# Performance work log

Measured on AMD Instinct MI355X. Metric: run time of the kernel, lower is better.

Reference implementation:

```python
import jax, jax.numpy as jnp
import numpy as np

B, N, N_IN, N_HID, EIN = 8, 256, 64, 128, 16


def setup_inputs() -> dict:
    key = jax.random.key(0)
    ks = jax.random.split(key, 12)
    s_in = 1.0 / np.sqrt(N_IN)
    s_e = 1.0 / np.sqrt(EIN)
    s_h = 1.0 / np.sqrt(N_HID)
    return {
        "x": jax.random.normal(ks[0], (B, N, N_IN), jnp.float32),
        "e": jax.random.normal(ks[1], (B, N, N, EIN), jnp.float32),
        "Wf": jax.random.uniform(ks[2], (N_IN, N_HID), jnp.float32, -s_in, s_in),
        "bf": jax.random.uniform(ks[3], (N_HID,), jnp.float32, -s_in, s_in),
        "Wt": jax.random.uniform(ks[4], (N_IN, N_HID), jnp.float32, -s_in, s_in),
        "bt": jax.random.uniform(ks[5], (N_HID,), jnp.float32, -s_in, s_in),
        "We": jax.random.uniform(ks[6], (EIN, N_HID), jnp.float32, -s_e, s_e),
        "be": jax.random.uniform(ks[7], (N_HID,), jnp.float32, -s_e, s_e),
        "W1": jax.random.uniform(ks[8], (N_HID, N_HID), jnp.float32, -s_h, s_h),
        "b1": jax.random.uniform(ks[9], (N_HID,), jnp.float32, -s_h, s_h),
        "W2": jax.random.uniform(ks[10], (N_HID, N_IN), jnp.float32, -s_h, s_h),
        "b2": jax.random.uniform(ks[11], (N_IN,), jnp.float32, -s_h, s_h),
    }


def reference(x, e, Wf, bf, Wt, bt, We, be, W1, b1, W2, b2):
    # x: [B,N,F], e: [B,N,N,E]
    n = x.shape[1]
    ne_f = x @ Wf + bf                      # [B,N,H] (node_emb_1)
    ne_t = x @ Wt + bt                      # [B,N,H] (node_emb_2)
    ee = e @ We + be                        # [B,N,N,H]
    # pair[b,i,j] = node_emb_1[b,j] + node_emb_2[b,i] + edge_emb[b,i,j]
    pair = ne_f[:, None, :, :] + ne_t[:, :, None, :] + ee
    # zero the diagonal (both node_emb and edge_emb diagonals were zeroed)
    mask = (1.0 - jnp.eye(n, dtype=x.dtype))[None, :, :, None]
    node_emb = jax.nn.relu(pair * mask).mean(axis=2)  # [B,N,H]
    h = jax.nn.relu(node_emb @ W1 + b1)
    return h @ W2 + b2 + x
```

## Files before the change

### kernel.cpp

```cpp
#include <hip/hip_runtime.h>
#include <hip/hip_bf16.h>


#define BB 8
#define NN 256
#define FF 64
#define HH 128
#define EE 16
#define NCH 5

typedef __attribute__((ext_vector_type(8))) short bf16x8;
typedef __attribute__((ext_vector_type(16))) float f32x16;

__device__ __forceinline__ short f2bf(float f) {
    union { float f; unsigned u; } v; v.f = f;
    unsigned r = v.u + 0x7FFFu + ((v.u >> 16) & 1u);
    return (short)(r >> 16);
}
__device__ __forceinline__ float bf2f(short s) {
    union { unsigned u; float f; } v; v.u = ((unsigned)(unsigned short)s) << 16;
    return v.f;
}
__device__ __forceinline__ unsigned pkbf(float lo, float hi) {
    unsigned r;
    asm("v_cvt_pk_bf16_f32 %0, %1, %2" : "=v"(r) : "v"(lo), "v"(hi));
    return r;
}
union bfu { bf16x8 v; unsigned u[4]; };

__global__ __launch_bounds__(128) void k_prep(
    const float* __restrict__ x, const float* __restrict__ Wt,
    const float* __restrict__ bf, const float* __restrict__ bt, const float* __restrict__ be,
    const float* __restrict__ We, const float* __restrict__ Wf,
    const float* __restrict__ W1, const float* __restrict__ W2,
    float* __restrict__ net, short* __restrict__ xbf,
    short* __restrict__ Bpack, short* __restrict__ W1p, short* __restrict__ W2p)
{
    __shared__ float smx[4 * FF];
    const int tid = threadIdx.x;
    const int row0 = blockIdx.x * 4;

    smx[tid]       = x[(size_t)row0 * FF + tid];
    smx[tid + 128] = x[(size_t)row0 * FF + tid + 128];
    __syncthreads();

    const int h = tid;
    const float bsum = bf[h] + bt[h] + be[h];
    float a0 = bsum, a1 = bsum, a2 = bsum, a3 = bsum;

    #pragma unroll 8
    for (int k = 0; k < FF; ++k) {
        const float wt = Wt[k * HH + h];
        a0 = fmaf(smx[k], wt, a0);
        a1 = fmaf(smx[FF + k], wt, a1);
        a2 = fmaf(smx[2 * FF + k], wt, a2);
        a3 = fmaf(smx[3 * FF + k], wt, a3);
    }
    net[(size_t)(row0 + 0) * HH + h] = a0;
    net[(size_t)(row0 + 1) * HH + h] = a1;
    net[(size_t)(row0 + 2) * HH + h] = a2;
    net[(size_t)(row0 + 3) * HH + h] = a3;

    const int r = tid >> 6, f = tid & 63;
    xbf[(size_t)(row0 + r) * FF + f]     = f2bf(smx[r * FF + f]);
    xbf[(size_t)(row0 + r + 2) * FF + f] = f2bf(smx[(r + 2) * FF + f]);

    if (blockIdx.x < 32) {
        for (int t = blockIdx.x * 128 + tid; t < 34816; t += 32 * 128) {
            if (t < 10240) {
                const int el = t & 7, lane = (t >> 3) & 63, ht = (t >> 9) & 3, ch = t >> 11;
                const int kl = 8 * (lane >> 5) + el;
                const int hh = ht * 32 + (lane & 31);
                Bpack[t] = f2bf(ch == 0 ? We[kl * HH + hh] : Wf[(16 * (ch - 1) + kl) * HH + hh]);
            } else if (t < 26624) {
                const int t2 = t - 10240;
                const int el = t2 & 7, lane = (t2 >> 3) & 63, ht = (t2 >> 9) & 3, ch = (t2 >> 11) & 7;
                const int k = 16 * ch + 8 * (lane >> 5) + el;
                const int hh = ht * 32 + (lane & 31);
                W1p[t2] = f2bf(W1[k * HH + hh]);
            } else {
                const int t3 = t - 26624;
                const int el = t3 & 7, lane = (t3 >> 3) & 63, ht = (t3 >> 9) & 1, ch = t3 >> 10;
                const int k = 16 * ch + 8 * (lane >> 5) + el;
                const int hh = ht * 32 + (lane & 31);
                W2p[t3] = f2bf(W2[k * FF + hh]);
            }
        }
    }
}

__global__ __launch_bounds__(256) void k_pair(
    const float* __restrict__ e, const float* __restrict__ net,
    const short* __restrict__ xbf, const short* __restrict__ Bpack,
    float* __restrict__ S)
{
    const int row  = blockIdx.x;
    const int b    = row >> 8;
    const int tid  = threadIdx.x;
    const int wave = tid >> 6;
    const int lane = tid & 63;
    const int c    = lane & 31;
    const int half = lane >> 5;

    const bf16x8* __restrict__ bp = (const bf16x8*)Bpack;
    bf16x8 bfrag[NCH];
    #pragma unroll
    for (int ch = 0; ch < NCH; ++ch)
        bfrag[ch] = bp[(ch * 4 + wave) * 64 + lane];

    const float netv = net[(size_t)row * HH + wave * 32 + c];

    const float* __restrict__ eRow = e + (size_t)row * (NN * EE);
    const short* __restrict__ xb   = xbf + (size_t)b * (NN * FF);

    float acc = 0.f;

    #pragma unroll 2
    for (int jt = 0; jt < 8; ++jt) {
        const int j = jt * 32 + c;

        const float4* ap = (const float4*)(eRow + (size_t)j * EE + 8 * half);
        const float4 p0 = ap[0];
        const float4 p1 = ap[1];
        bfu ae;
        ae.u[0] = pkbf(p0.x, p0.y);
        ae.u[1] = pkbf(p0.z, p0.w);
        ae.u[2] = pkbf(p1.x, p1.y);
        ae.u[3] = pkbf(p1.z, p1.w);

        const bf16x8* xp = (const bf16x8*)(xb + (size_t)j * FF + 8 * half);
        const bf16x8 ax0 = xp[0];
        const bf16x8 ax1 = xp[2];
        const bf16x8 ax2 = xp[4];
        const bf16x8 ax3 = xp[6];

        f32x16 d = {netv,netv,netv,netv, netv,netv,netv,netv,
                    netv,netv,netv,netv, netv,netv,netv,netv};
        d = __builtin_amdgcn_mfma_f32_32x32x16_bf16(ae.v, bfrag[0], d, 0, 0, 0);
        d = __builtin_amdgcn_mfma_f32_32x32x16_bf16(ax0,  bfrag[1], d, 0, 0, 0);
        d = __builtin_amdgcn_mfma_f32_32x32x16_bf16(ax1,  bfrag[2], d, 0, 0, 0);
        d = __builtin_amdgcn_mfma_f32_32x32x16_bf16(ax2,  bfrag[3], d, 0, 0, 0);
        d = __builtin_amdgcn_mfma_f32_32x32x16_bf16(ax3,  bfrag[4], d, 0, 0, 0);
        #pragma unroll
        for (int r = 0; r < 16; ++r) acc += fmaxf(d[r], 0.f);
    }

    acc += __shfl_xor(acc, 32);
    if (lane < 32) S[(size_t)row * HH + wave * 32 + c] = acc;
}

__global__ __launch_bounds__(256) void k_mlp(
    const float* __restrict__ x, const float* __restrict__ e,
    const float* __restrict__ S, const float* __restrict__ net,
    const short* __restrict__ xbf, const short* __restrict__ Bpack,
    const short* __restrict__ W1p, const short* __restrict__ W2p,
    const float* __restrict__ b1, const float* __restrict__ b2,
    float* __restrict__ out)
{
    const int row0 = blockIdx.x * 32;
    const int tid  = threadIdx.x;
    const int wave = tid >> 6;
    const int lane = tid & 63;
    const int c    = lane & 31;
    const int half = lane >> 5;

    __shared__ float Dt[32][132];
    __shared__ short neL[32][136];
    __shared__ short h1L[32][136];

    {
        const int gr = row0 + c;
        const int bb = gr >> 8, ii = gr & (NN - 1);
        const float* ed = e + ((size_t)(bb * NN + ii) * NN + ii) * EE + 8 * half;
        const float4 p0 = ((const float4*)ed)[0];
        const float4 p1 = ((const float4*)ed)[1];
        bfu ae;
        ae.u[0] = pkbf(p0.x, p0.y);
        ae.u[1] = pkbf(p0.z, p0.w);
        ae.u[2] = pkbf(p1.x, p1.y);
        ae.u[3] = pkbf(p1.z, p1.w);

        const bf16x8* xp = (const bf16x8*)(xbf + (size_t)gr * FF + 8 * half);
        const bf16x8 ax0 = xp[0];
        const bf16x8 ax1 = xp[2];
        const bf16x8 ax2 = xp[4];
        const bf16x8 ax3 = xp[6];

        const bf16x8* bp = (const bf16x8*)Bpack;
        f32x16 d = {0.f,0.f,0.f,0.f, 0.f,0.f,0.f,0.f, 0.f,0.f,0.f,0.f, 0.f,0.f,0.f,0.f};
        d = __builtin_amdgcn_mfma_f32_32x32x16_bf16(ae.v, bp[(0*4+wave)*64+lane], d, 0, 0, 0);
        d = __builtin_amdgcn_mfma_f32_32x32x16_bf16(ax0,  bp[(1*4+wave)*64+lane], d, 0, 0, 0);
        d = __builtin_amdgcn_mfma_f32_32x32x16_bf16(ax1,  bp[(2*4+wave)*64+lane], d, 0, 0, 0);
        d = __builtin_amdgcn_mfma_f32_32x32x16_bf16(ax2,  bp[(3*4+wave)*64+lane], d, 0, 0, 0);
        d = __builtin_amdgcn_mfma_f32_32x32x16_bf16(ax3,  bp[(4*4+wave)*64+lane], d, 0, 0, 0);
        #pragma unroll
        for (int r = 0; r < 16; ++r) {
            const int rowj = (r & 3) + 8 * (r >> 2) + 4 * half;
            Dt[rowj][wave * 32 + c] = d[r];
        }
    }
    __syncthreads();

    {
        const int r  = tid >> 3;
        const int h0 = (tid & 7) * 16;
        const size_t base = (size_t)(row0 + r) * HH + h0;
        unsigned uo[8];
        #pragma unroll
        for (int q = 0; q < 4; ++q) {
            const float4 sv = *(const float4*)&S[base + 4 * q];
            const float4 nv = *(const float4*)&net[base + 4 * q];
            const float4 dv = *(const float4*)&Dt[r][h0 + 4 * q];
            const float n0 = (sv.x - fmaxf(dv.x + nv.x, 0.f)) * (1.0f / NN);
            const float n1 = (sv.y - fmaxf(dv.y + nv.y, 0.f)) * (1.0f / NN);
            const float n2 = (sv.z - fmaxf(dv.z + nv.z, 0.f)) * (1.0f / NN);
            const float n3 = (sv.w - fmaxf(dv.w + nv.w, 0.f)) * (1.0f / NN);
            uo[2 * q]     = pkbf(n0, n1);
            uo[2 * q + 1] = pkbf(n2, n3);
        }
        uint4* dst = (uint4*)&neL[r][h0];
        dst[0] = make_uint4(uo[0], uo[1], uo[2], uo[3]);
        dst[1] = make_uint4(uo[4], uo[5], uo[6], uo[7]);
    }
    __syncthreads();

    {
        const float b1v = b1[wave * 32 + c];
        const bf16x8* wp = (const bf16x8*)W1p;
        f32x16 d = {b1v,b1v,b1v,b1v, b1v,b1v,b1v,b1v, b1v,b1v,b1v,b1v, b1v,b1v,b1v,b1v};
        #pragma unroll
        for (int ch = 0; ch < 8; ++ch) {
            const bf16x8 a = *(const bf16x8*)&neL[c][16 * ch + 8 * half];
            d = __builtin_amdgcn_mfma_f32_32x32x16_bf16(a, wp[(ch * 4 + wave) * 64 + lane], d, 0, 0, 0);
        }
        #pragma unroll
        for (int r = 0; r < 16; ++r) {
            const int rowj = (r & 3) + 8 * (r >> 2) + 4 * half;
            h1L[rowj][wave * 32 + c] = f2bf(fmaxf(d[r], 0.f));
        }
    }
    __syncthreads();

    if (wave < 2) {
        const float b2v = b2[wave * 32 + c];
        const bf16x8* wp = (const bf16x8*)W2p;
        f32x16 d = {b2v,b2v,b2v,b2v, b2v,b2v,b2v,b2v, b2v,b2v,b2v,b2v, b2v,b2v,b2v,b2v};
        #pragma unroll
        for (int ch = 0; ch < 8; ++ch) {
            const bf16x8 a = *(const bf16x8*)&h1L[c][16 * ch + 8 * half];
            d = __builtin_amdgcn_mfma_f32_32x32x16_bf16(a, wp[(ch * 2 + wave) * 64 + lane], d, 0, 0, 0);
        }
        #pragma unroll
        for (int r = 0; r < 16; ++r) {
            const int rowj = (r & 3) + 8 * (r >> 2) + 4 * half;
            const size_t idx = (size_t)(row0 + rowj) * FF + wave * 32 + c;
            out[idx] = d[r] + x[idx];
        }
    }
}

extern "C" void kernel_launch(void* const* d_in, const int* in_sizes, int n_in,
                              void* d_out, int out_size, void* d_ws, size_t ws_size,
                              hipStream_t stream) {
    (void)in_sizes; (void)n_in; (void)out_size; (void)ws_size;
    const float* x  = (const float*)d_in[0];
    const float* e  = (const float*)d_in[1];
    const float* Wf = (const float*)d_in[2];
    const float* bf = (const float*)d_in[3];
    const float* Wt = (const float*)d_in[4];
    const float* bt = (const float*)d_in[5];
    const float* We = (const float*)d_in[6];
    const float* be = (const float*)d_in[7];
    const float* W1 = (const float*)d_in[8];
    const float* b1 = (const float*)d_in[9];
    const float* W2 = (const float*)d_in[10];
    const float* b2 = (const float*)d_in[11];
    float* out = (float*)d_out;

    char* w = (char*)d_ws;
    float* net   = (float*)w;                 w += (size_t)BB * NN * HH * 4;
    float* Sbuf  = (float*)w;                 w += (size_t)BB * NN * HH * 4;
    short* xbf   = (short*)w;                 w += (size_t)BB * NN * FF * 2;
    short* Bpack = (short*)w;                 w += NCH * 4 * 64 * 8 * 2;
    short* W1p   = (short*)w;                 w += 8 * 4 * 64 * 8 * 2;
    short* W2p   = (short*)w;

    k_prep<<<(BB * NN) / 4, 128, 0, stream>>>(x, Wt, bf, bt, be, We, Wf, W1, W2,
                                              net, xbf, Bpack, W1p, W2p);
    k_pair<<<BB * NN, 256, 0, stream>>>(e, net, xbf, Bpack, Sbuf);
    k_mlp<<<(BB * NN) / 32, 256, 0, stream>>>(x, e, Sbuf, net, xbf, Bpack, W1p, W2p,
                                              b1, b2, out);
}
```

Before: 138.5 us.

## Stage edge rows through double-buffered LDS and prepack x into MFMA layout

In k_pair, the edge tile is no longer loaded redundantly by all four waves and converted per wave. The block now loads it cooperatively once, converts it to bf16 and stores it in a double-buffered LDS tile, prefetching the next j-tile while the MFMAs run. k_prep also writes a second copy of x in bf16, pre-swizzled into MFMA fragment order, so the x operand loads are contiguous per lane. The ReLU-sum reduction is split across four accumulators. The cost is a __syncthreads per iteration and extra workspace and writes in k_prep.

```diff
diff --git a/kernel.cpp b/kernel.cpp
--- a/kernel.cpp
+++ b/kernel.cpp
@@ -33,7 +33,7 @@
     const float* __restrict__ bf, const float* __restrict__ bt, const float* __restrict__ be,
     const float* __restrict__ We, const float* __restrict__ Wf,
     const float* __restrict__ W1, const float* __restrict__ W2,
-    float* __restrict__ net, short* __restrict__ xbf,
+    float* __restrict__ net, short* __restrict__ xbf, short* __restrict__ xbfp,
     short* __restrict__ Bpack, short* __restrict__ W1p, short* __restrict__ W2p)
 {
     __shared__ float smx[4 * FF];
@@ -61,9 +61,28 @@
     net[(size_t)(row0 + 2) * HH + h] = a2;
     net[(size_t)(row0 + 3) * HH + h] = a3;
 
-    const int r = tid >> 6, f = tid & 63;
-    xbf[(size_t)(row0 + r) * FF + f]     = f2bf(smx[r * FF + f]);
-    xbf[(size_t)(row0 + r + 2) * FF + f] = f2bf(smx[(r + 2) * FF + f]);
+    {
+        const int r = tid >> 6, f = tid & 63;
+        xbf[(size_t)(row0 + r) * FF + f]     = f2bf(smx[r * FF + f]);
+        xbf[(size_t)(row0 + r + 2) * FF + f] = f2bf(smx[(r + 2) * FF + f]);
+    }
+
+    {
+        const int r    = tid >> 5;
+        const int q    = tid & 31;
+        const int ch   = q >> 3;
+        const int half = (q >> 2) & 1;
+        const int el2  = q & 3;
+        const int gj   = row0 + r;
+        const int bb   = gj >> 8;
+        const int jj   = gj & 255;
+        const int jt   = jj >> 5;
+        const int cc   = jj & 31;
+        const float lo = smx[r * FF + ch * 16 + half * 8 + el2 * 2];
+        const float hi = smx[r * FF + ch * 16 + half * 8 + el2 * 2 + 1];
+        ((unsigned*)xbfp)[((((size_t)bb * 8 + jt) * 4 + ch) * 64 + half * 32 + cc) * 4 + el2]
+            = pkbf(lo, hi);
+    }
 
     if (blockIdx.x < 32) {
         for (int t = blockIdx.x * 128 + tid; t < 34816; t += 32 * 128) {
@@ -91,7 +110,7 @@
 
 __global__ __launch_bounds__(256) void k_pair(
     const float* __restrict__ e, const float* __restrict__ net,
-    const short* __restrict__ xbf, const short* __restrict__ Bpack,
+    const short* __restrict__ xbfp, const short* __restrict__ Bpack,
     float* __restrict__ S)
 {
     const int row  = blockIdx.x;
@@ -102,6 +121,8 @@
     const int c    = lane & 31;
     const int half = lane >> 5;
 
+    __shared__ __align__(16) char eL[2][1024];
+
     const bf16x8* __restrict__ bp = (const bf16x8*)Bpack;
     bf16x8 bfrag[NCH];
     #pragma unroll
@@ -111,40 +132,50 @@
     const float netv = net[(size_t)row * HH + wave * 32 + c];
 
     const float* __restrict__ eRow = e + (size_t)row * (NN * EE);
-    const short* __restrict__ xb   = xbf + (size_t)b * (NN * FF);
-
-    float acc = 0.f;
+    const bf16x8* __restrict__ xq  = (const bf16x8*)(xbfp + (size_t)b * 8 * 4 * 512);
+
+    const int sc   = tid >> 3;
+    const int sk2  = tid & 7;
+    const int edst = ((sk2 >> 2) * 128 + sc * 4 + (sk2 & 3)) * 4;
+
+    float2 ev = *(const float2*)(eRow + (size_t)tid * 2);
+    *(unsigned*)(&eL[0][edst]) = pkbf(ev.x, ev.y);
+    __syncthreads();
+
+    float acc0 = 0.f, acc1 = 0.f, acc2 = 0.f, acc3 = 0.f;
 
     #pragma unroll 2
     for (int jt = 0; jt < 8; ++jt) {
-        const int j = jt * 32 + c;
-
-        const float4* ap = (const float4*)(eRow + (size_t)j * EE + 8 * half);
-        const float4 p0 = ap[0];
-        const float4 p1 = ap[1];
-        bfu ae;
-        ae.u[0] = pkbf(p0.x, p0.y);
-        ae.u[1] = pkbf(p0.z, p0.w);
-        ae.u[2] = pkbf(p1.x, p1.y);
-        ae.u[3] = pkbf(p1.z, p1.w);
-
-        const bf16x8* xp = (const bf16x8*)(xb + (size_t)j * FF + 8 * half);
-        const bf16x8 ax0 = xp[0];
-        const bf16x8 ax1 = xp[2];
-        const bf16x8 ax2 = xp[4];
-        const bf16x8 ax3 = xp[6];
+        const int buf = jt & 1;
+        if (jt < 7) ev = *(const float2*)(eRow + (size_t)(jt + 1) * 512 + tid * 2);
+
+        const bf16x8 ae  = *(const bf16x8*)(&eL[buf][half * 512 + c * 16]);
+        const bf16x8 ax0 = xq[((size_t)jt * 4 + 0) * 64 + lane];
+        const bf16x8 ax1 = xq[((size_t)jt * 4 + 1) * 64 + lane];
+        const bf16x8 ax2 = xq[((size_t)jt * 4 + 2) * 64 + lane];
+        const bf16x8 ax3 = xq[((size_t)jt * 4 + 3) * 64 + lane];
 
         f32x16 d = {netv,netv,netv,netv, netv,netv,netv,netv,
                     netv,netv,netv,netv, netv,netv,netv,netv};
-        d = __builtin_amdgcn_mfma_f32_32x32x16_bf16(ae.v, bfrag[0], d, 0, 0, 0);
-        d = __builtin_amdgcn_mfma_f32_32x32x16_bf16(ax0,  bfrag[1], d, 0, 0, 0);
-        d = __builtin_amdgcn_mfma_f32_32x32x16_bf16(ax1,  bfrag[2], d, 0, 0, 0);
-        d = __builtin_amdgcn_mfma_f32_32x32x16_bf16(ax2,  bfrag[3], d, 0, 0, 0);
-        d = __builtin_amdgcn_mfma_f32_32x32x16_bf16(ax3,  bfrag[4], d, 0, 0, 0);
-        #pragma unroll
-        for (int r = 0; r < 16; ++r) acc += fmaxf(d[r], 0.f);
-    }
-
+        d = __builtin_amdgcn_mfma_f32_32x32x16_bf16(ae,  bfrag[0], d, 0, 0, 0);
+        d = __builtin_amdgcn_mfma_f32_32x32x16_bf16(ax0, bfrag[1], d, 0, 0, 0);
+        d = __builtin_amdgcn_mfma_f32_32x32x16_bf16(ax1, bfrag[2], d, 0, 0, 0);
+        d = __builtin_amdgcn_mfma_f32_32x32x16_bf16(ax2, bfrag[3], d, 0, 0, 0);
+        d = __builtin_amdgcn_mfma_f32_32x32x16_bf16(ax3, bfrag[4], d, 0, 0, 0);
+
+        if (jt < 7) *(unsigned*)(&eL[buf ^ 1][edst]) = pkbf(ev.x, ev.y);
+
+        #pragma unroll
+        for (int r = 0; r < 16; r += 4) {
+            acc0 += fmaxf(d[r + 0], 0.f);
+            acc1 += fmaxf(d[r + 1], 0.f);
+            acc2 += fmaxf(d[r + 2], 0.f);
+            acc3 += fmaxf(d[r + 3], 0.f);
+        }
+        __syncthreads();
+    }
+
+    float acc = (acc0 + acc1) + (acc2 + acc3);
     acc += __shfl_xor(acc, 32);
     if (lane < 32) S[(size_t)row * HH + wave * 32 + c] = acc;
 }
@@ -281,13 +312,14 @@
     float* net   = (float*)w;                 w += (size_t)BB * NN * HH * 4;
     float* Sbuf  = (float*)w;                 w += (size_t)BB * NN * HH * 4;
     short* xbf   = (short*)w;                 w += (size_t)BB * NN * FF * 2;
+    short* xbfp  = (short*)w;                 w += (size_t)BB * NN * FF * 2;
     short* Bpack = (short*)w;                 w += NCH * 4 * 64 * 8 * 2;
     short* W1p   = (short*)w;                 w += 8 * 4 * 64 * 8 * 2;
     short* W2p   = (short*)w;
 
     k_prep<<<(BB * NN) / 4, 128, 0, stream>>>(x, Wt, bf, bt, be, We, Wf, W1, W2,
-                                              net, xbf, Bpack, W1p, W2p);
-    k_pair<<<BB * NN, 256, 0, stream>>>(e, net, xbf, Bpack, Sbuf);
+                                              net, xbf, xbfp, Bpack, W1p, W2p);
+    k_pair<<<BB * NN, 256, 0, stream>>>(e, net, xbfp, Bpack, Sbuf);
     k_mlp<<<(BB * NN) / 32, 256, 0, stream>>>(x, e, Sbuf, net, xbf, Bpack, W1p, W2p,
                                               b1, b2, out);
 }
```

After: 122.4 us. 1.13x faster.
